# Optimization experiments

Hardware: AMD Instinct MI355X
Metric: run time of the kernel (lower is better)

## Reference

```python
import jax, jax.numpy as jnp
import numpy as np

B, N, E, D_IN, D_OUT = 8, 8192, 131072, 128, 128
LN_EPS = 1e-5

def setup_inputs() -> dict:
    key = jax.random.key(0)
    k1, k2, k3, k4 = jax.random.split(key, 4)
    node_features = jax.random.normal(k1, (B, N, D_IN), dtype=jnp.float32)
    edge_index = jax.random.randint(k2, (B, 2, E), 0, N, dtype=jnp.int64)
    node_mask = jnp.ones((B, N), dtype=jnp.float32)
    # Linear params (torch Linear: y = x @ W.T + b)
    W = jax.random.normal(k3, (D_OUT, D_IN), dtype=jnp.float32) / np.sqrt(D_IN)
    b = jax.random.normal(k4, (D_OUT,), dtype=jnp.float32) * 0.01
    # LayerNorm params
    gamma = jnp.ones((D_OUT,), dtype=jnp.float32)
    beta = jnp.zeros((D_OUT,), dtype=jnp.float32)
    return {"node_features": node_features, "edge_index": edge_index,
            "node_mask": node_mask, "W": W, "b": b, "gamma": gamma, "beta": beta}

def reference(node_features, edge_index, node_mask, W, b, gamma, beta):
    max_nodes = node_features.shape[1]
    h = jnp.einsum('bni,oi->bno', node_features, W) + b  # [B,N,D_OUT]
    def agg_one(hb, eb):
        # gather source features then scatter-add into targets
        return jax.ops.segment_sum(hb[eb[0]], eb[1], num_segments=max_nodes)
    aggregated = jax.vmap(agg_one)(h, edge_index)  # [B,N,D_OUT]
    h = h + aggregated / jnp.sqrt(jnp.float32(max_nodes))
    # dropout is identity in eval mode
    mu = jnp.mean(h, axis=-1, keepdims=True)
    var = jnp.mean((h - mu) ** 2, axis=-1, keepdims=True)
    h = (h - mu) * jax.lax.rsqrt(var + LN_EPS) * gamma + beta
    h = jax.nn.relu(h)
    return h * node_mask[..., None]
```

## Files before the change

kernel.cpp:

```cpp
#include <hip/hip_runtime.h>

#define B_ 8
#define N_ 8192
#define E_ 131072
#define D_ 128
#define M_ (B_ * N_)
#define SLOTS 64
#define FWIN 512
constexpr float INV_SQRT_N = 0.011048543456039806f;
constexpr float LN_EPS_C = 1e-5f;

typedef __attribute__((ext_vector_type(8))) short bf16x8;
typedef __attribute__((ext_vector_type(4))) float f32x4;
typedef __attribute__((ext_vector_type(4))) float f32x4v;
typedef __attribute__((ext_vector_type(4))) unsigned u32x4;

static __device__ __forceinline__ unsigned short f2bf(float f) {
  unsigned u = __float_as_uint(f);
  u += 0x7fffu + ((u >> 16) & 1u);
  return (unsigned short)(u >> 16);
}
static __device__ __forceinline__ float bflo(unsigned u) {
  return __uint_as_float(u << 16);
}
static __device__ __forceinline__ float bfhi(unsigned u) {
  return __uint_as_float(u & 0xffff0000u);
}
static __device__ __forceinline__ bf16x8 cvt8v(const f32x4v a, const f32x4v b) {
  bf16x8 r;
  r[0] = (short)f2bf(a.x); r[1] = (short)f2bf(a.y);
  r[2] = (short)f2bf(a.z); r[3] = (short)f2bf(a.w);
  r[4] = (short)f2bf(b.x); r[5] = (short)f2bf(b.y);
  r[6] = (short)f2bf(b.z); r[7] = (short)f2bf(b.w);
  return r;
}

__global__ __launch_bounds__(1024, 4) void gemm_fill_kernel(
    const float* __restrict__ X, const float* __restrict__ W,
    const float* __restrict__ bias, const int* __restrict__ eidx,
    int* __restrict__ cnt, unsigned short* __restrict__ bucket,
    unsigned short* __restrict__ hb) {
  __shared__ unsigned cnt_l[FWIN];
  __shared__ unsigned short bkt_l[FWIN * SLOTS];
  if (blockIdx.x < 128) {
    const int wave = threadIdx.x >> 6;
    const int lane = threadIdx.x & 63;
    const int m16 = lane & 15;
    const int q = lane >> 4;
    const int hf = wave & 1;
    const int ng = wave >> 1;

    bf16x8 wf[4][4];
#pragma unroll
    for (int kt4 = 0; kt4 < 4; ++kt4) {
#pragma unroll
      for (int tt = 0; tt < 4; ++tt) {
        const float* wr = W + (size_t)(hf * 64 + tt * 16 + m16) * D_ +
                          kt4 * 32 + q * 8;
        wf[kt4][tt] = cvt8v(*(const f32x4v*)wr, *(const f32x4v*)(wr + 4));
      }
    }

    const int nbase0 = blockIdx.x * 512 + ng * 64;
#pragma unroll 2
    for (int s = 0; s < 4; ++s) {
      const int nbase = nbase0 + s * 16;
      const float* xrow = X + (size_t)(nbase + m16) * D_;

      f32x4 acc[4];
#pragma unroll
      for (int tt = 0; tt < 4; ++tt) acc[tt] = (f32x4){0.f, 0.f, 0.f, 0.f};

#pragma unroll
      for (int kt4 = 0; kt4 < 4; ++kt4) {
        const f32x4v xa = __builtin_nontemporal_load(
            (const f32x4v*)(xrow + kt4 * 32 + q * 8));
        const f32x4v xb = __builtin_nontemporal_load(
            (const f32x4v*)(xrow + kt4 * 32 + q * 8 + 4));
        const bf16x8 xf = cvt8v(xa, xb);
#pragma unroll
        for (int tt = 0; tt < 4; ++tt) {
          acc[tt] = __builtin_amdgcn_mfma_f32_16x16x32_bf16(wf[kt4][tt], xf,
                                                            acc[tt], 0, 0, 0);
        }
      }

      const size_t orow = (size_t)(nbase + m16) * D_;
#pragma unroll
      for (int tt = 0; tt < 4; ++tt) {
        const int f0 = hf * 64 + tt * 16 + q * 4;
        const float4 b4 = *(const float4*)&bias[f0];
        uint2 uu;
        uu.x = (unsigned)f2bf(acc[tt][0] + b4.x) |
               ((unsigned)f2bf(acc[tt][1] + b4.y) << 16);
        uu.y = (unsigned)f2bf(acc[tt][2] + b4.z) |
               ((unsigned)f2bf(acc[tt][3] + b4.w) << 16);
        *(uint2*)(hb + orow + f0) = uu;
      }
    }
  } else {
    const int f = blockIdx.x - 128;
    const int batch = f & 7;
    const int w = f >> 3;
    const int t = threadIdx.x;
    const int wbase = w * FWIN;

    if (t < FWIN) cnt_l[t] = 0u;
    __syncthreads();

    const int* __restrict__ srcp = eidx + batch * 2 * E_;
    const int* __restrict__ tgtp = srcp + E_;

#define PROC4(tv, sv)                                                   \
  {                                                                     \
    const unsigned l0 = (unsigned)(tv.x - wbase);                       \
    const unsigned l1 = (unsigned)(tv.y - wbase);                       \
    const unsigned l2 = (unsigned)(tv.z - wbase);                       \
    const unsigned l3 = (unsigned)(tv.w - wbase);                       \
    unsigned p0 = 0xffffu, p1 = 0xffffu, p2 = 0xffffu, p3 = 0xffffu;    \
    if (l0 < FWIN) p0 = atomicAdd(&cnt_l[l0], 1u);                      \
    if (l1 < FWIN) p1 = atomicAdd(&cnt_l[l1], 1u);                      \
    if (l2 < FWIN) p2 = atomicAdd(&cnt_l[l2], 1u);                      \
    if (l3 < FWIN) p3 = atomicAdd(&cnt_l[l3], 1u);                      \
    if (p0 < SLOTS) bkt_l[l0 * SLOTS + p0] = (unsigned short)sv.x;      \
    if (p1 < SLOTS) bkt_l[l1 * SLOTS + p1] = (unsigned short)sv.y;      \
    if (p2 < SLOTS) bkt_l[l2 * SLOTS + p2] = (unsigned short)sv.z;      \
    if (p3 < SLOTS) bkt_l[l3 * SLOTS + p3] = (unsigned short)sv.w;      \
  }

    int e = t * 8;
    int4 ct0 = *(const int4*)(tgtp + e);
    int4 ct1 = *(const int4*)(tgtp + e + 4);
    int4 cs0 = *(const int4*)(srcp + e);
    int4 cs1 = *(const int4*)(srcp + e + 4);
#pragma unroll 1
    for (int it = 0; it < 15; ++it) {
      const int en = e + 8192;
      const int4 nt0 = *(const int4*)(tgtp + en);
      const int4 nt1 = *(const int4*)(tgtp + en + 4);
      const int4 ns0 = *(const int4*)(srcp + en);
      const int4 ns1 = *(const int4*)(srcp + en + 4);
      PROC4(ct0, cs0);
      PROC4(ct1, cs1);
      ct0 = nt0; ct1 = nt1; cs0 = ns0; cs1 = ns1;
      e = en;
    }
    PROC4(ct0, cs0);
    PROC4(ct1, cs1);
#undef PROC4
    __syncthreads();

    const int nodebase = batch * N_ + wbase;
    if (t < FWIN) cnt[nodebase + t] = (int)cnt_l[t];
    const u32x4* ls = (const u32x4*)bkt_l;
    u32x4* gd = (u32x4*)(bucket + (size_t)nodebase * SLOTS);
#pragma unroll
    for (int i = 0; i < (FWIN * SLOTS * 2) / (16 * 1024); ++i)
      gd[i * 1024 + t] = ls[i * 1024 + t];
  }
}

__global__ __launch_bounds__(256, 8) void gather_finalize_kernel(
    const unsigned short* __restrict__ hb, const unsigned short* __restrict__ bucket,
    const int* __restrict__ cnt, const float* __restrict__ mask,
    const float* __restrict__ gamma, const float* __restrict__ beta,
    float* __restrict__ out) {
  const int bid = blockIdx.x;
  const int batch = bid & 7;
  const int wave = threadIdx.x >> 6;
  const int lane = threadIdx.x & 63;
  const int g = lane >> 4;
  const int c = lane & 15;
  const int r = (bid >> 3) * 16 + wave * 4 + g;
  const int row = batch * N_ + r;

  const u32x4* hub4 = (const u32x4*)hb + (size_t)batch * N_ * 16;

  const int deg = min(cnt[row], SLOTS);
  const uint2 su = *(const uint2*)&bucket[(size_t)row * SLOTS + c * 4];
  const u32x4 ur = hub4[r * 16 + c];
  const float m = mask[row];

  float a[8];
#pragma unroll
  for (int k = 0; k < 8; ++k) a[k] = 0.f;

  int jb = 0;
  for (; jb + 8 <= deg; jb += 8) {
    const int L = jb >> 2;
    const unsigned w0 = (unsigned)__shfl((int)su.x, L, 16);
    const unsigned w1 = (unsigned)__shfl((int)su.y, L, 16);
    const unsigned w2 = (unsigned)__shfl((int)su.x, L + 1, 16);
    const unsigned w3 = (unsigned)__shfl((int)su.y, L + 1, 16);
    const int idx[8] = {(int)(w0 & 0xffff), (int)(w0 >> 16),
                        (int)(w1 & 0xffff), (int)(w1 >> 16),
                        (int)(w2 & 0xffff), (int)(w2 >> 16),
                        (int)(w3 & 0xffff), (int)(w3 >> 16)};
    u32x4 v[8];
#pragma unroll
    for (int i = 0; i < 8; ++i) v[i] = hub4[idx[i] * 16 + c];
#pragma unroll
    for (int i = 0; i < 8; ++i) {
      a[0] += bflo(v[i].x); a[1] += bfhi(v[i].x);
      a[2] += bflo(v[i].y); a[3] += bfhi(v[i].y);
      a[4] += bflo(v[i].z); a[5] += bfhi(v[i].z);
      a[6] += bflo(v[i].w); a[7] += bfhi(v[i].w);
    }
  }
  for (; jb < deg; ++jb) {
    const int L = jb >> 2;
    const unsigned w = ((jb >> 1) & 1) ? (unsigned)__shfl((int)su.y, L, 16)
                                       : (unsigned)__shfl((int)su.x, L, 16);
    const int idx = (jb & 1) ? (int)(w >> 16) : (int)(w & 0xffff);
    const u32x4 v = hub4[idx * 16 + c];
    a[0] += bflo(v.x); a[1] += bfhi(v.x);
    a[2] += bflo(v.y); a[3] += bfhi(v.y);
    a[4] += bflo(v.z); a[5] += bfhi(v.z);
    a[6] += bflo(v.w); a[7] += bfhi(v.w);
  }

  float x[8];
  x[0] = bflo(ur.x) + a[0] * INV_SQRT_N;
  x[1] = bfhi(ur.x) + a[1] * INV_SQRT_N;
  x[2] = bflo(ur.y) + a[2] * INV_SQRT_N;
  x[3] = bfhi(ur.y) + a[3] * INV_SQRT_N;
  x[4] = bflo(ur.z) + a[4] * INV_SQRT_N;
  x[5] = bfhi(ur.z) + a[5] * INV_SQRT_N;
  x[6] = bflo(ur.w) + a[6] * INV_SQRT_N;
  x[7] = bfhi(ur.w) + a[7] * INV_SQRT_N;

  float s0 = 0.f, ss = 0.f;
#pragma unroll
  for (int k = 0; k < 8; ++k) {
    s0 += x[k];
    ss += x[k] * x[k];
  }
#pragma unroll
  for (int o = 8; o >= 1; o >>= 1) {
    s0 += __shfl_xor(s0, o, 16);
    ss += __shfl_xor(ss, o, 16);
  }
  const float mu = s0 * (1.f / 128.f);
  float var = ss * (1.f / 128.f) - mu * mu;
  var = var < 0.f ? 0.f : var;
  const float rstd = rsqrtf(var + LN_EPS_C);

  const f32x4v g0 = *((const f32x4v*)gamma + c * 2);
  const f32x4v g1 = *((const f32x4v*)gamma + c * 2 + 1);
  const f32x4v b0 = *((const f32x4v*)beta + c * 2);
  const f32x4v b1 = *((const f32x4v*)beta + c * 2 + 1);

  f32x4v o0, o1;
  o0.x = (x[0] - mu) * rstd * g0.x + b0.x;
  o0.y = (x[1] - mu) * rstd * g0.y + b0.y;
  o0.z = (x[2] - mu) * rstd * g0.z + b0.z;
  o0.w = (x[3] - mu) * rstd * g0.w + b0.w;
  o1.x = (x[4] - mu) * rstd * g1.x + b1.x;
  o1.y = (x[5] - mu) * rstd * g1.y + b1.y;
  o1.z = (x[6] - mu) * rstd * g1.z + b1.z;
  o1.w = (x[7] - mu) * rstd * g1.w + b1.w;
  o0.x = (o0.x > 0.f ? o0.x : 0.f) * m;
  o0.y = (o0.y > 0.f ? o0.y : 0.f) * m;
  o0.z = (o0.z > 0.f ? o0.z : 0.f) * m;
  o0.w = (o0.w > 0.f ? o0.w : 0.f) * m;
  o1.x = (o1.x > 0.f ? o1.x : 0.f) * m;
  o1.y = (o1.y > 0.f ? o1.y : 0.f) * m;
  o1.z = (o1.z > 0.f ? o1.z : 0.f) * m;
  o1.w = (o1.w > 0.f ? o1.w : 0.f) * m;

  f32x4v* op = (f32x4v*)out + (size_t)row * 32 + c * 2;
  __builtin_nontemporal_store(o0, op);
  __builtin_nontemporal_store(o1, op + 1);
}

extern "C" void kernel_launch(void* const* d_in, const int* in_sizes, int n_in,
                              void* d_out, int out_size, void* d_ws,
                              size_t ws_size, hipStream_t stream) {
  const float* X = (const float*)d_in[0];
  const int* eidx = (const int*)d_in[1];
  const float* mask = (const float*)d_in[2];
  const float* W = (const float*)d_in[3];
  const float* bias = (const float*)d_in[4];
  const float* gamma = (const float*)d_in[5];
  const float* beta = (const float*)d_in[6];
  float* out = (float*)d_out;

  unsigned short* hb = (unsigned short*)d_ws;
  unsigned short* bucket = hb + (size_t)M_ * D_;
  int* cnt = (int*)(bucket + (size_t)M_ * SLOTS);


  gemm_fill_kernel<<<256, 1024, 0, stream>>>(X, W, bias, eidx, cnt,
                                             bucket, hb);
  gather_finalize_kernel<<<M_ / 16, 256, 0, stream>>>(hb, bucket, cnt, mask,
                                                      gamma, beta, out);
}
```

Baseline: 166.4 us.

## Compact in-window edges with wave ballot queue before bucket fill

The bucket-fill blocks now scan target indices with a wave ballot and push the matching edges, packed as local node and edge offset, into a per-wave LDS queue. A second pass then processes only the queued edges. It loads their source indices on demand and runs dense shared-memory atomics. This removes the unconditional source-index loads and the heavily predicated, divergent atomic work across all edges. The cost is 48KB of extra LDS per block, which the GEMM blocks also allocate, plus gather-style source reads. The queue has no overflow check, so it relies on each wave seeing fewer than 768 matches.

```diff
diff --git a/kernel.cpp b/kernel.cpp
--- a/kernel.cpp
+++ b/kernel.cpp
@@ -7,6 +7,7 @@
 #define M_ (B_ * N_)
 #define SLOTS 64
 #define FWIN 512
+#define QCAP 768
 constexpr float INV_SQRT_N = 0.011048543456039806f;
 constexpr float LN_EPS_C = 1e-5f;
 
@@ -34,6 +35,10 @@
   r[6] = (short)f2bf(b.z); r[7] = (short)f2bf(b.w);
   return r;
 }
+static __device__ __forceinline__ unsigned lanepos(unsigned long long m) {
+  return __builtin_amdgcn_mbcnt_hi(
+      (unsigned)(m >> 32), __builtin_amdgcn_mbcnt_lo((unsigned)m, 0u));
+}
 
 __global__ __launch_bounds__(1024, 4) void gemm_fill_kernel(
     const float* __restrict__ X, const float* __restrict__ W,
@@ -42,6 +47,7 @@
     unsigned short* __restrict__ hb) {
   __shared__ unsigned cnt_l[FWIN];
   __shared__ unsigned short bkt_l[FWIN * SLOTS];
+  __shared__ unsigned q_l[16 * QCAP];
   if (blockIdx.x < 128) {
     const int wave = threadIdx.x >> 6;
     const int lane = threadIdx.x & 63;
@@ -103,6 +109,8 @@
     const int batch = f & 7;
     const int w = f >> 3;
     const int t = threadIdx.x;
+    const int wave = t >> 6;
+    const int lane = t & 63;
     const int wbase = w * FWIN;
 
     if (t < FWIN) cnt_l[t] = 0u;
@@ -111,43 +119,56 @@
     const int* __restrict__ srcp = eidx + batch * 2 * E_;
     const int* __restrict__ tgtp = srcp + E_;
 
-#define PROC4(tv, sv)                                                   \
-  {                                                                     \
-    const unsigned l0 = (unsigned)(tv.x - wbase);                       \
-    const unsigned l1 = (unsigned)(tv.y - wbase);                       \
-    const unsigned l2 = (unsigned)(tv.z - wbase);                       \
-    const unsigned l3 = (unsigned)(tv.w - wbase);                       \
-    unsigned p0 = 0xffffu, p1 = 0xffffu, p2 = 0xffffu, p3 = 0xffffu;    \
-    if (l0 < FWIN) p0 = atomicAdd(&cnt_l[l0], 1u);                      \
-    if (l1 < FWIN) p1 = atomicAdd(&cnt_l[l1], 1u);                      \
-    if (l2 < FWIN) p2 = atomicAdd(&cnt_l[l2], 1u);                      \
-    if (l3 < FWIN) p3 = atomicAdd(&cnt_l[l3], 1u);                      \
-    if (p0 < SLOTS) bkt_l[l0 * SLOTS + p0] = (unsigned short)sv.x;      \
-    if (p1 < SLOTS) bkt_l[l1 * SLOTS + p1] = (unsigned short)sv.y;      \
-    if (p2 < SLOTS) bkt_l[l2 * SLOTS + p2] = (unsigned short)sv.z;      \
-    if (p3 < SLOTS) bkt_l[l3 * SLOTS + p3] = (unsigned short)sv.w;      \
+    unsigned* __restrict__ qw = q_l + wave * QCAP;
+    unsigned qn = 0;
+
+#define SCAN1(tval, eoff)                                            \
+  {                                                                  \
+    const unsigned l_ = (unsigned)((tval)-wbase);                    \
+    const bool m_ = l_ < FWIN;                                       \
+    const unsigned long long bal_ = __ballot(m_);                    \
+    if (m_) qw[qn + lanepos(bal_)] = (l_ << 17) | (unsigned)(eoff);  \
+    qn += (unsigned)__popcll(bal_);                                  \
   }
 
     int e = t * 8;
     int4 ct0 = *(const int4*)(tgtp + e);
     int4 ct1 = *(const int4*)(tgtp + e + 4);
-    int4 cs0 = *(const int4*)(srcp + e);
-    int4 cs1 = *(const int4*)(srcp + e + 4);
 #pragma unroll 1
     for (int it = 0; it < 15; ++it) {
       const int en = e + 8192;
       const int4 nt0 = *(const int4*)(tgtp + en);
       const int4 nt1 = *(const int4*)(tgtp + en + 4);
-      const int4 ns0 = *(const int4*)(srcp + en);
-      const int4 ns1 = *(const int4*)(srcp + en + 4);
-      PROC4(ct0, cs0);
-      PROC4(ct1, cs1);
-      ct0 = nt0; ct1 = nt1; cs0 = ns0; cs1 = ns1;
+      SCAN1(ct0.x, e); SCAN1(ct0.y, e + 1);
+      SCAN1(ct0.z, e + 2); SCAN1(ct0.w, e + 3);
+      SCAN1(ct1.x, e + 4); SCAN1(ct1.y, e + 5);
+      SCAN1(ct1.z, e + 6); SCAN1(ct1.w, e + 7);
+      ct0 = nt0; ct1 = nt1;
       e = en;
     }
-    PROC4(ct0, cs0);
-    PROC4(ct1, cs1);
-#undef PROC4
+    SCAN1(ct0.x, e); SCAN1(ct0.y, e + 1);
+    SCAN1(ct0.z, e + 2); SCAN1(ct0.w, e + 3);
+    SCAN1(ct1.x, e + 4); SCAN1(ct1.y, e + 5);
+    SCAN1(ct1.z, e + 6); SCAN1(ct1.w, e + 7);
+#undef SCAN1
+
+    unsigned j = lane;
+    for (; j + 64 < qn; j += 128) {
+      const unsigned v0 = qw[j];
+      const unsigned v1 = qw[j + 64];
+      const unsigned short s0 = (unsigned short)srcp[v0 & 0x1FFFFu];
+      const unsigned short s1 = (unsigned short)srcp[v1 & 0x1FFFFu];
+      const unsigned p0 = atomicAdd(&cnt_l[v0 >> 17], 1u);
+      const unsigned p1 = atomicAdd(&cnt_l[v1 >> 17], 1u);
+      if (p0 < SLOTS) bkt_l[(v0 >> 17) * SLOTS + p0] = s0;
+      if (p1 < SLOTS) bkt_l[(v1 >> 17) * SLOTS + p1] = s1;
+    }
+    if (j < qn) {
+      const unsigned v = qw[j];
+      const unsigned short s = (unsigned short)srcp[v & 0x1FFFFu];
+      const unsigned p = atomicAdd(&cnt_l[v >> 17], 1u);
+      if (p < SLOTS) bkt_l[(v >> 17) * SLOTS + p] = s;
+    }
     __syncthreads();
 
     const int nodebase = batch * N_ + wbase;
```

After: 162.4 us. -2.4%, faster.
